# Optimization experiments

Measured on AMD Instinct MI355X. Metric: run time of the kernel, lower is better.

## Reference

```python
import jax, jax.numpy as jnp
import numpy as np

N_NODES = 40000
N_EDGES = 640000
D_FEAT = 128


def setup_inputs() -> dict:
    key = jax.random.key(0)
    k1, k2, k3 = jax.random.split(key, 3)
    feats = jax.random.normal(k1, (N_NODES, D_FEAT), dtype=jnp.float32)
    src = jax.random.randint(k2, (N_EDGES,), 0, N_NODES, dtype=jnp.int32)
    dst = jax.random.randint(k3, (N_EDGES,), 0, N_NODES, dtype=jnp.int32)
    return {"feats": feats, "src": src, "dst": dst}


def reference(feats, src, dst):
    n = feats.shape[0]
    # gather node features to edges and take L1 diff: u_sub_v then sum(|.|)
    diff = feats[src] - feats[dst]                                # [E, D]
    e = jnp.exp(-0.01 * jnp.sum(jnp.abs(diff), axis=-1))          # [E], exp(-1/100 * L1)
    # edge softmax grouped by destination node (numerically stable)
    m = jax.ops.segment_max(e, dst, num_segments=n)               # [N]
    ex = jnp.exp(e - m[dst])                                      # [E]
    s = jax.ops.segment_sum(ex, dst, num_segments=n)              # [N]
    out = ex / s[dst]                                             # [E]
    return out[:, None]                                           # [E, 1] (matches feats.view(-1,1,D) head dim)
```

## Files before the change

kernel.cpp:

```cpp
#include <hip/hip_runtime.h>
#include <math.h>

#define D_FEAT 128

__global__ __launch_bounds__(256) void prep_kernel(
    const float* __restrict__ feats, unsigned int* __restrict__ q8,
    float* __restrict__ s, int n_nodes, int n_vec)
{
    int i = blockIdx.x * blockDim.x + threadIdx.x;
    if (i < n_nodes) s[i] = 0.0f;
    if (i < n_vec) {
        const float4* fp = (const float4*)feats;
        float4 a = fp[2 * i];
        float4 b = fp[2 * i + 1];
        #define Q(x) ((unsigned int)(int)(rintf(fminf(fmaxf((x) * 24.0f, -127.0f), 127.0f)) + 128.0f))
        unsigned int w0 = Q(a.x) | (Q(a.y) << 8) | (Q(a.z) << 16) | (Q(a.w) << 24);
        unsigned int w1 = Q(b.x) | (Q(b.y) << 8) | (Q(b.z) << 16) | (Q(b.w) << 24);
        #undef Q
        ((uint2*)q8)[i] = make_uint2(w0, w1);
    }
}

__global__ __launch_bounds__(256) void edge_kernel(
    const unsigned int* __restrict__ q8, const int* __restrict__ src,
    const int* __restrict__ dst, float* __restrict__ out,
    float* __restrict__ s, int n_edges)
{
    int tid = blockIdx.x * blockDim.x + threadIdx.x;
    int l   = tid & 7;
    int e   = tid >> 3;
    if (e >= n_edges) return;

    int sr = src[e], dr = dst[e];
    const uint4* t = (const uint4*)q8;
    uint4 a = t[(size_t)sr * 8 + l];
    uint4 b = t[(size_t)dr * 8 + l];

    unsigned int acc = 0;
    acc = __builtin_amdgcn_sad_u8(a.x, b.x, acc);
    acc = __builtin_amdgcn_sad_u8(a.y, b.y, acc);
    acc = __builtin_amdgcn_sad_u8(a.z, b.z, acc);
    acc = __builtin_amdgcn_sad_u8(a.w, b.w, acc);

    int p = (int)acc;
    p += __shfl_xor(p, 4);
    p += __shfl_xor(p, 2);
    p += __shfl_xor(p, 1);

    if (l == 0) {
        float w = expf(expf((float)p * (-1.0f / 2400.0f)));
        out[e] = w;
        atomicAdd(s + dr, w);
    }
}

__global__ void norm_kernel(const int* __restrict__ dst, const float* __restrict__ s,
                            float* __restrict__ out, int n_edges)
{
    int i = blockIdx.x * blockDim.x + threadIdx.x;
    if (i >= n_edges) return;
    out[i] = out[i] / s[dst[i]];
}

extern "C" void kernel_launch(void* const* d_in, const int* in_sizes, int n_in,
                              void* d_out, int out_size, void* d_ws, size_t ws_size,
                              hipStream_t stream) {
    const float* feats = (const float*)d_in[0];
    const int*   src   = (const int*)d_in[1];
    const int*   dst   = (const int*)d_in[2];
    float* out = (float*)d_out;

    int n_edges = in_sizes[1];
    int n_nodes = in_sizes[0] / D_FEAT;
    int n_vec   = n_nodes * (D_FEAT / 8);

    float* sseg = (float*)d_ws;
    unsigned int* q8 = (unsigned int*)((char*)d_ws + (size_t)n_nodes * sizeof(float));

    prep_kernel<<<(n_vec + 255) / 256, 256, 0, stream>>>(feats, q8, sseg, n_nodes, n_vec);

    long long threads = (long long)n_edges * 8;
    int n_blocks_edge = (int)((threads + 255) / 256);
    edge_kernel<<<n_blocks_edge, 256, 0, stream>>>(q8, src, dst, out, sseg, n_edges);

    norm_kernel<<<(n_edges + 255) / 256, 256, 0, stream>>>(dst, sseg, out, n_edges);
}
```

Baseline: 111.4 us.

## Fuse prep, edge and normalize into one cooperative kernel with split atomics

Replaces three kernel launches with one cooperative persistent kernel that uses grid-wide syncs between quantization, edge-weight accumulation and normalization. Segment sums are spread over four slots per node, indexed by edge parity, to reduce atomic contention, and normalization reads them as float4 and processes four edges per thread. This removes launch gaps but adds grid barrier cost and limits the grid to occupancy-bound persistence. A fallback path keeps the three-kernel version if cooperative launch fails.

```diff
diff --git a/kernel.cpp b/kernel.cpp
--- a/kernel.cpp
+++ b/kernel.cpp
@@ -1,65 +1,126 @@
 #include <hip/hip_runtime.h>
+#include <hip/hip_cooperative_groups.h>
 #include <math.h>
+
+namespace cg = cooperative_groups;
 
 #define D_FEAT 128
 
+__device__ __forceinline__ unsigned int quant8(float x) {
+    return (unsigned int)(int)(rintf(fminf(fmaxf(x * 24.0f, -127.0f), 127.0f)) + 128.0f);
+}
+
+__device__ __forceinline__ void quant_vec8(const float4* __restrict__ fp,
+                                           uint2* __restrict__ qv, int i) {
+    float4 a = fp[2 * i];
+    float4 b = fp[2 * i + 1];
+    unsigned int w0 = quant8(a.x) | (quant8(a.y) << 8) | (quant8(a.z) << 16) | (quant8(a.w) << 24);
+    unsigned int w1 = quant8(b.x) | (quant8(b.y) << 8) | (quant8(b.z) << 16) | (quant8(b.w) << 24);
+    qv[i] = make_uint2(w0, w1);
+}
+
+__device__ __forceinline__ float edge_weight(const uint4* __restrict__ t,
+                                             int sr, int dr, int l) {
+    uint4 a = t[(size_t)sr * 8 + l];
+    uint4 b = t[(size_t)dr * 8 + l];
+    unsigned int acc = 0;
+    acc = __builtin_amdgcn_sad_u8(a.x, b.x, acc);
+    acc = __builtin_amdgcn_sad_u8(a.y, b.y, acc);
+    acc = __builtin_amdgcn_sad_u8(a.z, b.z, acc);
+    acc = __builtin_amdgcn_sad_u8(a.w, b.w, acc);
+    int p = (int)acc;
+    p += __shfl_xor(p, 4);
+    p += __shfl_xor(p, 2);
+    p += __shfl_xor(p, 1);
+    return expf(expf((float)p * (-1.0f / 2400.0f)));
+}
+
+__global__ __launch_bounds__(256, 8) void fused_kernel(
+    const float* __restrict__ feats, const int* __restrict__ src,
+    const int* __restrict__ dst, float* __restrict__ out,
+    unsigned int* __restrict__ q8, float* __restrict__ s4,
+    int n_nodes, int n_edges)
+{
+    const int tid = blockIdx.x * blockDim.x + threadIdx.x;
+    const int nthreads = gridDim.x * blockDim.x;
+
+    for (int i = tid; i < n_nodes * 4; i += nthreads) s4[i] = 0.0f;
+    const int n_vec = n_nodes * (D_FEAT / 8);
+    const float4* fp = (const float4*)feats;
+    uint2* qv = (uint2*)q8;
+    for (int i = tid; i < n_vec; i += nthreads) quant_vec8(fp, qv, i);
+
+    cg::this_grid().sync();
+
+    const int l = tid & 7;
+    const int g = tid >> 3;
+    const int ngroups = nthreads >> 3;
+    const uint4* t = (const uint4*)q8;
+    for (int e = g; e < n_edges; e += ngroups) {
+        int sr = src[e], dr = dst[e];
+        float w = edge_weight(t, sr, dr, l);
+        if (l == 0) {
+            out[e] = w;
+            atomicAdd(s4 + (size_t)dr * 4 + (e & 3), w);
+        }
+    }
+
+    cg::this_grid().sync();
+
+    const int n4 = n_edges >> 2;
+    const float4* s4v = (const float4*)s4;
+    for (int i = tid; i < n4; i += nthreads) {
+        int4 d4 = ((const int4*)dst)[i];
+        float4 w4 = ((const float4*)out)[i];
+        float4 a = s4v[d4.x];
+        float4 b = s4v[d4.y];
+        float4 c = s4v[d4.z];
+        float4 d = s4v[d4.w];
+        w4.x /= (a.x + a.y) + (a.z + a.w);
+        w4.y /= (b.x + b.y) + (b.z + b.w);
+        w4.z /= (c.x + c.y) + (c.z + c.w);
+        w4.w /= (d.x + d.y) + (d.z + d.w);
+        ((float4*)out)[i] = w4;
+    }
+    for (int e = (n4 << 2) + tid; e < n_edges; e += nthreads) {
+        float4 sv = s4v[dst[e]];
+        out[e] = out[e] / ((sv.x + sv.y) + (sv.z + sv.w));
+    }
+}
+
 __global__ __launch_bounds__(256) void prep_kernel(
     const float* __restrict__ feats, unsigned int* __restrict__ q8,
-    float* __restrict__ s, int n_nodes, int n_vec)
+    float* __restrict__ s4, int n_nodes, int n_vec)
 {
     int i = blockIdx.x * blockDim.x + threadIdx.x;
-    if (i < n_nodes) s[i] = 0.0f;
-    if (i < n_vec) {
-        const float4* fp = (const float4*)feats;
-        float4 a = fp[2 * i];
-        float4 b = fp[2 * i + 1];
-        #define Q(x) ((unsigned int)(int)(rintf(fminf(fmaxf((x) * 24.0f, -127.0f), 127.0f)) + 128.0f))
-        unsigned int w0 = Q(a.x) | (Q(a.y) << 8) | (Q(a.z) << 16) | (Q(a.w) << 24);
-        unsigned int w1 = Q(b.x) | (Q(b.y) << 8) | (Q(b.z) << 16) | (Q(b.w) << 24);
-        #undef Q
-        ((uint2*)q8)[i] = make_uint2(w0, w1);
-    }
+    if (i < n_nodes * 4) s4[i] = 0.0f;
+    if (i < n_vec) quant_vec8((const float4*)feats, (uint2*)q8, i);
 }
 
 __global__ __launch_bounds__(256) void edge_kernel(
     const unsigned int* __restrict__ q8, const int* __restrict__ src,
     const int* __restrict__ dst, float* __restrict__ out,
-    float* __restrict__ s, int n_edges)
+    float* __restrict__ s4, int n_edges)
 {
     int tid = blockIdx.x * blockDim.x + threadIdx.x;
-    int l   = tid & 7;
-    int e   = tid >> 3;
+    int l = tid & 7;
+    int e = tid >> 3;
     if (e >= n_edges) return;
-
     int sr = src[e], dr = dst[e];
-    const uint4* t = (const uint4*)q8;
-    uint4 a = t[(size_t)sr * 8 + l];
-    uint4 b = t[(size_t)dr * 8 + l];
-
-    unsigned int acc = 0;
-    acc = __builtin_amdgcn_sad_u8(a.x, b.x, acc);
-    acc = __builtin_amdgcn_sad_u8(a.y, b.y, acc);
-    acc = __builtin_amdgcn_sad_u8(a.z, b.z, acc);
-    acc = __builtin_amdgcn_sad_u8(a.w, b.w, acc);
-
-    int p = (int)acc;
-    p += __shfl_xor(p, 4);
-    p += __shfl_xor(p, 2);
-    p += __shfl_xor(p, 1);
-
+    float w = edge_weight((const uint4*)q8, sr, dr, l);
     if (l == 0) {
-        float w = expf(expf((float)p * (-1.0f / 2400.0f)));
         out[e] = w;
-        atomicAdd(s + dr, w);
+        atomicAdd(s4 + (size_t)dr * 4 + (e & 3), w);
     }
 }
 
-__global__ void norm_kernel(const int* __restrict__ dst, const float* __restrict__ s,
+__global__ void norm_kernel(const int* __restrict__ dst, const float* __restrict__ s4,
                             float* __restrict__ out, int n_edges)
 {
     int i = blockIdx.x * blockDim.x + threadIdx.x;
     if (i >= n_edges) return;
-    out[i] = out[i] / s[dst[i]];
+    float4 sv = ((const float4*)s4)[dst[i]];
+    out[i] = out[i] / ((sv.x + sv.y) + (sv.z + sv.w));
 }
 
 extern "C" void kernel_launch(void* const* d_in, const int* in_sizes, int n_in,
@@ -74,14 +135,32 @@
     int n_nodes = in_sizes[0] / D_FEAT;
     int n_vec   = n_nodes * (D_FEAT / 8);
 
-    float* sseg = (float*)d_ws;
-    unsigned int* q8 = (unsigned int*)((char*)d_ws + (size_t)n_nodes * sizeof(float));
+    float* s4 = (float*)d_ws;
+    unsigned int* q8 = (unsigned int*)((char*)d_ws + (size_t)n_nodes * 4 * sizeof(float));
 
-    prep_kernel<<<(n_vec + 255) / 256, 256, 0, stream>>>(feats, q8, sseg, n_nodes, n_vec);
+    static int grid_blocks = 0;
+    if (grid_blocks == 0) {
+        int bpc = 0;
+        (void)hipOccupancyMaxActiveBlocksPerMultiprocessor(&bpc, (const void*)fused_kernel, 256, 0);
+        if (bpc < 1) bpc = 1;
+        if (bpc > 8) bpc = 8;
+        int ncu = 256;
+        hipDeviceProp_t prop;
+        if (hipGetDeviceProperties(&prop, 0) == hipSuccess && prop.multiProcessorCount > 0)
+            ncu = prop.multiProcessorCount;
+        grid_blocks = bpc * ncu;
+    }
 
-    long long threads = (long long)n_edges * 8;
-    int n_blocks_edge = (int)((threads + 255) / 256);
-    edge_kernel<<<n_blocks_edge, 256, 0, stream>>>(q8, src, dst, out, sseg, n_edges);
-
-    norm_kernel<<<(n_edges + 255) / 256, 256, 0, stream>>>(dst, sseg, out, n_edges);
+    void* args[] = { (void*)&feats, (void*)&src, (void*)&dst, (void*)&out,
+                     (void*)&q8, (void*)&s4, (void*)&n_nodes, (void*)&n_edges };
+    hipError_t err = hipLaunchCooperativeKernel((const void*)fused_kernel,
+                                                dim3(grid_blocks), dim3(256),
+                                                args, 0, stream);
+    if (err != hipSuccess) {
+        int thr0 = n_nodes * 4 > n_vec ? n_nodes * 4 : n_vec;
+        prep_kernel<<<(thr0 + 255) / 256, 256, 0, stream>>>(feats, q8, s4, n_nodes, n_vec);
+        long long threads = (long long)n_edges * 8;
+        edge_kernel<<<(int)((threads + 255) / 256), 256, 0, stream>>>(q8, src, dst, out, s4, n_edges);
+        norm_kernel<<<(n_edges + 255) / 256, 256, 0, stream>>>(dst, s4, out, n_edges);
+    }
 }
```

New measurement: 438.7 us. 3.94x slower.
